# Kernel tuning notes

Measured on AMD Instinct MI355X. Metric: run time of the kernel, lower is better.

## Reference

```python
import jax, jax.numpy as jnp
import numpy as np

N, D_IN, H, D_EMB = 2048, 128, 256, 64


def setup_inputs() -> dict:
    key = jax.random.key(0)
    ks = jax.random.split(key, 8)
    x = jax.random.normal(ks[0], (N, D_IN), dtype=jnp.float32)
    adj = jnp.zeros((N, N), dtype=jnp.float32)  # only its last dim is used (eye sizing)
    s = 0.05
    W0 = jax.random.normal(ks[1], (D_IN, H), dtype=jnp.float32) * s
    b0 = jnp.zeros((H,), dtype=jnp.float32)
    W1 = jax.random.normal(ks[2], (H, D_EMB), dtype=jnp.float32) * s
    b1 = jnp.zeros((D_EMB,), dtype=jnp.float32)
    W2 = jax.random.normal(ks[3], (D_IN, D_IN), dtype=jnp.float32) * s
    b2 = jnp.zeros((D_IN,), dtype=jnp.float32)
    temp = jnp.float32(0.1)
    theta = jnp.float32(0.1)
    return {"x": x, "adj": adj, "W0": W0, "b0": b0, "W1": W1, "b1": b1,
            "W2": W2, "b2": b2, "temp": temp, "theta": theta}


def reference(x, adj, W0, b0, W1, b1, W2, b2, temp, theta):
    # layer 0 (on x) and middle layer 1 (on out_x), both with ReLU activation
    out_x = jax.nn.relu(x @ W0 + b0)            # [N, H]
    emb = jax.nn.relu(out_x @ W1 + b1)          # [N, D_EMB]
    # last layer is applied to the ORIGINAL x (per the `x = model(x)` branch)
    x_last = x @ W2 + b2                        # [N, D_IN]

    # dist[i,j] = -||emb_i - emb_j||^2, computed via the gemm expansion
    sq = jnp.sum(emb * emb, axis=1)             # [N]
    dist = -(sq[:, None] + sq[None, :] - 2.0 * (emb @ emb.T))  # [N, N]

    prob = jax.nn.sigmoid((1.0 + temp) * dist + (5.0 + theta))
    A = prob + jnp.eye(adj.shape[-1], dtype=prob.dtype)        # [N, N]

    # diag(A.sum(-1))^{-1} @ A @ x_last  ==  rowwise divide by degree
    deg = jnp.sum(A, axis=-1)                   # [N]
    out = jax.nn.relu((A @ x_last) / deg[:, None])

    # sigmoid(.) > 0 everywhere, so all N*N entries are nonzero: adj_wts is the
    # full flattened adjacency (data-independent shape, jit-safe)
    adj_wts = A.reshape(-1)
    return out, adj_wts
```

## Files before the change

kernel.cpp:

```cpp
#include <hip/hip_runtime.h>
#include <hip/hip_bf16.h>


typedef short bf16x8 __attribute__((ext_vector_type(8)));
typedef float f32x4 __attribute__((ext_vector_type(4)));

__device__ __forceinline__ unsigned short f2bf(float f) {
    unsigned u = __float_as_uint(f);
    unsigned r = u + 0x7fffu + ((u >> 16) & 1u);
    return (unsigned short)(r >> 16);
}

__device__ __forceinline__ bf16x8 pack_rne8(const float* p) {
    union { unsigned u[4]; bf16x8 v; } r;
    #pragma unroll
    for (int i = 0; i < 4; ++i) {
        unsigned lo = __float_as_uint(p[2 * i]) + 0x8000u;
        unsigned hi = __float_as_uint(p[2 * i + 1]) + 0x8000u;
        r.u[i] = __builtin_amdgcn_perm(hi, lo, 0x07060302u);
    }
    return r.v;
}

__device__ __forceinline__ bf16x8 pack_bf8(const float* p) {
    union { unsigned u[4]; bf16x8 v; } r;
    #pragma unroll
    for (int i = 0; i < 4; ++i)
        r.u[i] = __builtin_amdgcn_perm(__float_as_uint(p[2 * i + 1]),
                                       __float_as_uint(p[2 * i]), 0x07060302u);
    return r.v;
}

__global__ __launch_bounds__(256) void k1_mfma(
    const float* __restrict__ x,
    const float* __restrict__ W0, const float* __restrict__ b0,
    const float* __restrict__ W1, const float* __restrict__ b1,
    const float* __restrict__ W2, const float* __restrict__ b2,
    unsigned short* __restrict__ emb_bf,
    unsigned short* __restrict__ xlT_bf,
    float* __restrict__ sq)
{
    constexpr int LDO = 264;
    __shared__ unsigned short oxb[16 * LDO];
    __shared__ float sqs[4][16];

    const int t = threadIdx.x;
    const int lane = t & 63;
    const int w = t >> 6;
    const int m = lane & 15;
    const int q = lane >> 4;
    const int i0 = blockIdx.x * 16;

    bf16x8 ax[4];
    #pragma unroll
    for (int kb = 0; kb < 4; ++kb) {
        float xf[8];
        *(f32x4*)&xf[0] = *(const f32x4*)(x + (size_t)(i0 + m) * 128 + kb * 32 + q * 8);
        *(f32x4*)&xf[4] = *(const f32x4*)(x + (size_t)(i0 + m) * 128 + kb * 32 + q * 8 + 4);
        ax[kb] = pack_rne8(xf);
    }

    #pragma unroll
    for (int hh = 0; hh < 4; ++hh) {
        const int h = (w * 4 + hh) * 16 + m;
        float bb = b0[h];
        f32x4 acc = {bb, bb, bb, bb};
        #pragma unroll
        for (int kb = 0; kb < 4; ++kb) {
            float wf[8];
            #pragma unroll
            for (int j = 0; j < 8; ++j) wf[j] = W0[(size_t)(kb * 32 + q * 8 + j) * 256 + h];
            acc = __builtin_amdgcn_mfma_f32_16x16x32_bf16(ax[kb], pack_rne8(wf), acc, 0, 0, 0);
        }
        #pragma unroll
        for (int r = 0; r < 4; ++r)
            oxb[(q * 4 + r) * LDO + h] = f2bf(fmaxf(acc[r], 0.0f));
    }
    __syncthreads();

    {
        const int h = w * 16 + m;
        float bb = b1[h];
        f32x4 acc = {bb, bb, bb, bb};
        #pragma unroll
        for (int kb = 0; kb < 8; ++kb) {
            bf16x8 af = *(const bf16x8*)(&oxb[m * LDO + kb * 32 + q * 8]);
            float wf[8];
            #pragma unroll
            for (int j = 0; j < 8; ++j) wf[j] = W1[(size_t)(kb * 32 + q * 8 + j) * 64 + h];
            acc = __builtin_amdgcn_mfma_f32_16x16x32_bf16(af, pack_rne8(wf), acc, 0, 0, 0);
        }
        float s2[4];
        #pragma unroll
        for (int r = 0; r < 4; ++r) {
            float e = fmaxf(acc[r], 0.0f);
            emb_bf[(size_t)(i0 + q * 4 + r) * 64 + h] = f2bf(e);
            s2[r] = e * e;
        }
        #pragma unroll
        for (int r = 0; r < 4; ++r) {
            float v = s2[r];
            v += __shfl_xor(v, 1);
            v += __shfl_xor(v, 2);
            v += __shfl_xor(v, 4);
            v += __shfl_xor(v, 8);
            if (m == 0) sqs[w][q * 4 + r] = v;
        }
    }

    #pragma unroll
    for (int hh = 0; hh < 2; ++hh) {
        const int c = (w * 2 + hh) * 16 + m;
        float bb = b2[c];
        f32x4 acc = {bb, bb, bb, bb};
        #pragma unroll
        for (int kb = 0; kb < 4; ++kb) {
            float wf[8];
            #pragma unroll
            for (int j = 0; j < 8; ++j) wf[j] = W2[(size_t)(kb * 32 + q * 8 + j) * 128 + c];
            acc = __builtin_amdgcn_mfma_f32_16x16x32_bf16(ax[kb], pack_rne8(wf), acc, 0, 0, 0);
        }
        uint2 pk;
        pk.x = (unsigned)f2bf(acc[0]) | ((unsigned)f2bf(acc[1]) << 16);
        pk.y = (unsigned)f2bf(acc[2]) | ((unsigned)f2bf(acc[3]) << 16);
        *(uint2*)(&xlT_bf[(size_t)c * 2048 + i0 + q * 4]) = pk;
    }
    __syncthreads();
    if (t < 16)
        sq[i0 + t] = sqs[0][t] + sqs[1][t] + sqs[2][t] + sqs[3][t];
}

__global__ __launch_bounds__(256) void k2f(
    const unsigned short* __restrict__ emb_bf,
    const unsigned short* __restrict__ xlT_bf,
    const float* __restrict__ sq,
    const float* __restrict__ tempp, const float* __restrict__ thetap,
    float* __restrict__ adjw,
    float* __restrict__ outPart,
    float* __restrict__ degPart)
{
    constexpr int LDP = 132;
    __shared__ float Pt[2][16 * LDP];
    __shared__ float degS[4][16];

    const int t = threadIdx.x;
    const int lane = t & 63;
    const int w = t >> 6;
    const int m = lane & 15;
    const int q = lane >> 4;
    const int i0 = blockIdx.x * 16;
    const int bj = blockIdx.y;
    const int jstrip0 = bj * 256;
    const float scale = 1.0f + tempp[0];
    const float bias = 5.0f + thetap[0];

    bf16x8 a0 = *(const bf16x8*)(emb_bf + (size_t)(i0 + m) * 64 + q * 8);
    bf16x8 a1 = *(const bf16x8*)(emb_bf + (size_t)(i0 + m) * 64 + 32 + q * 8);
    float sqIr[4];
    #pragma unroll
    for (int r = 0; r < 4; ++r) sqIr[r] = sq[i0 + q * 4 + r];

    f32x4 accO0 = {0.f, 0.f, 0.f, 0.f};
    f32x4 accO1 = {0.f, 0.f, 0.f, 0.f};
    float dega[4] = {0.f, 0.f, 0.f, 0.f};
    const int cg = w * 32;

    #pragma unroll
    for (int jt = 0; jt < 2; ++jt) {
        const int j0 = jstrip0 + jt * 128;
        float* P = &Pt[jt][0];

        #pragma unroll
        for (int s = 0; s < 2; ++s) {
            const int col = (w * 2 + s) * 16 + m;
            const unsigned short* ebj = emb_bf + (size_t)(j0 + col) * 64;
            bf16x8 b0 = *(const bf16x8*)(ebj + q * 8);
            bf16x8 b1 = *(const bf16x8*)(ebj + 32 + q * 8);
            f32x4 S = {0.f, 0.f, 0.f, 0.f};
            S = __builtin_amdgcn_mfma_f32_16x16x32_bf16(a0, b0, S, 0, 0, 0);
            S = __builtin_amdgcn_mfma_f32_16x16x32_bf16(a1, b1, S, 0, 0, 0);

            const float csqJ = sq[j0 + col];
            const int gcol = j0 + col;
            #pragma unroll
            for (int r = 0; r < 4; ++r) {
                int grow = i0 + q * 4 + r;
                float dist = 2.0f * S[r] - sqIr[r] - csqJ;
                float z = scale * dist + bias;
                float p = 1.0f / (1.0f + __expf(-z));
                if (grow == gcol) p += 1.0f;
                dega[r] += p;
                P[(q * 4 + r) * LDP + col] = p;
            }
        }
        __syncthreads();

        {
            int row = t >> 4;
            int c0 = (t & 15) * 8;
            f32x4 v0 = *(const f32x4*)(&P[row * LDP + c0]);
            f32x4 v1 = *(const f32x4*)(&P[row * LDP + c0 + 4]);
            f32x4* dst = (f32x4*)(adjw + (size_t)(i0 + row) * 2048 + j0 + c0);
            __builtin_nontemporal_store(v0, dst);
            __builtin_nontemporal_store(v1, dst + 1);
        }

        #pragma unroll
        for (int s = 0; s < 4; ++s) {
            float af[8];
            *(f32x4*)(&af[0]) = *(const f32x4*)(&P[m * LDP + s * 32 + q * 8]);
            *(f32x4*)(&af[4]) = *(const f32x4*)(&P[m * LDP + s * 32 + q * 8 + 4]);
            bf16x8 aa = pack_bf8(af);
            const int k = j0 + s * 32 + q * 8;
            bf16x8 b0 = *(const bf16x8*)(xlT_bf + (size_t)(cg + m) * 2048 + k);
            bf16x8 b1 = *(const bf16x8*)(xlT_bf + (size_t)(cg + 16 + m) * 2048 + k);
            accO0 = __builtin_amdgcn_mfma_f32_16x16x32_bf16(aa, b0, accO0, 0, 0, 0);
            accO1 = __builtin_amdgcn_mfma_f32_16x16x32_bf16(aa, b1, accO1, 0, 0, 0);
        }
    }

    #pragma unroll
    for (int r = 0; r < 4; ++r) {
        float v = dega[r];
        v += __shfl_xor(v, 1);
        v += __shfl_xor(v, 2);
        v += __shfl_xor(v, 4);
        v += __shfl_xor(v, 8);
        if (m == 0) degS[w][q * 4 + r] = v;
    }
    __syncthreads();
    if (t < 16)
        degPart[bj * 2048 + i0 + t] =
            degS[0][t] + degS[1][t] + degS[2][t] + degS[3][t];

    float* op = outPart + ((size_t)bj * 2048 + i0) * 128;
    #pragma unroll
    for (int r = 0; r < 4; ++r) {
        op[(q * 4 + r) * 128 + cg + m] = accO0[r];
        op[(q * 4 + r) * 128 + cg + 16 + m] = accO1[r];
    }
}

__global__ __launch_bounds__(256) void k3_fin(
    const float* __restrict__ outPart, const float* __restrict__ degPart,
    float* __restrict__ out)
{
    int idx4 = (blockIdx.x * 256 + threadIdx.x) * 4;
    int row = idx4 >> 7;
    float4 s = make_float4(0.f, 0.f, 0.f, 0.f);
    float d = 0.f;
    #pragma unroll
    for (int p = 0; p < 8; ++p) {
        float4 v = *(const float4*)(&outPart[(size_t)p * 262144 + idx4]);
        s.x += v.x; s.y += v.y; s.z += v.z; s.w += v.w;
        d += degPart[p * 2048 + row];
    }
    float dinv = 1.0f / d;
    s.x = fmaxf(s.x * dinv, 0.f);
    s.y = fmaxf(s.y * dinv, 0.f);
    s.z = fmaxf(s.z * dinv, 0.f);
    s.w = fmaxf(s.w * dinv, 0.f);
    *(float4*)(&out[idx4]) = s;
}

extern "C" void kernel_launch(void* const* d_in, const int* in_sizes, int n_in,
                              void* d_out, int out_size, void* d_ws, size_t ws_size,
                              hipStream_t stream) {
    const float* x     = (const float*)d_in[0];
    const float* W0    = (const float*)d_in[2];
    const float* b0    = (const float*)d_in[3];
    const float* W1    = (const float*)d_in[4];
    const float* b1    = (const float*)d_in[5];
    const float* W2    = (const float*)d_in[6];
    const float* b2    = (const float*)d_in[7];
    const float* temp  = (const float*)d_in[8];
    const float* theta = (const float*)d_in[9];

    char* ws = (char*)d_ws;
    unsigned short* emb_bf = (unsigned short*)(ws);
    unsigned short* xlT_bf = (unsigned short*)(ws + 262144);
    float* sq      = (float*)(ws + 786432);
    float* degPart = (float*)(ws + 794624);
    float* outPart = (float*)(ws + 860160);

    float* out  = (float*)d_out;
    float* adjw = (float*)d_out + 262144;

    k1_mfma<<<128, 256, 0, stream>>>(x, W0, b0, W1, b1, W2, b2,
                                     emb_bf, xlT_bf, sq);
    k2f<<<dim3(128, 8), 256, 0, stream>>>(emb_bf, xlT_bf, sq, temp, theta,
                                          adjw, outPart, degPart);
    k3_fin<<<256, 256, 0, stream>>>(outPart, degPart, out);
}
```

Baseline: 113.4 us.

## Fuse final reduction into k2 via last-block atomic counter; widen k1 to 512 threads

Removes the separate k3_fin launch by having the last of the eight column-strip blocks for each row tile (found through an atomic counter zeroed in k1) sum the partial outputs and degrees and write the normalized ReLU output. k1 now runs eight waves per block: layer-0 work is split across all waves, and the W1 and W2 GEMMs run on separate wave groups so they proceed concurrently. This trades one kernel launch plus a full pass over outPart for threadfence and atomic overhead at the tail of k2, and it depends on k1 resetting the counters before every run.

```diff
diff --git a/kernel.cpp b/kernel.cpp
--- a/kernel.cpp
+++ b/kernel.cpp
@@ -31,14 +31,15 @@
     return r.v;
 }
 
-__global__ __launch_bounds__(256) void k1_mfma(
+__global__ __launch_bounds__(512) void k1_mfma(
     const float* __restrict__ x,
     const float* __restrict__ W0, const float* __restrict__ b0,
     const float* __restrict__ W1, const float* __restrict__ b1,
     const float* __restrict__ W2, const float* __restrict__ b2,
     unsigned short* __restrict__ emb_bf,
     unsigned short* __restrict__ xlT_bf,
-    float* __restrict__ sq)
+    float* __restrict__ sq,
+    int* __restrict__ cnt)
 {
     constexpr int LDO = 264;
     __shared__ unsigned short oxb[16 * LDO];
@@ -51,6 +52,8 @@
     const int q = lane >> 4;
     const int i0 = blockIdx.x * 16;
 
+    if (blockIdx.x == 0 && t < 128) cnt[t] = 0;
+
     bf16x8 ax[4];
     #pragma unroll
     for (int kb = 0; kb < 4; ++kb) {
@@ -61,8 +64,8 @@
     }
 
     #pragma unroll
-    for (int hh = 0; hh < 4; ++hh) {
-        const int h = (w * 4 + hh) * 16 + m;
+    for (int hh = 0; hh < 2; ++hh) {
+        const int h = (w * 2 + hh) * 16 + m;
         float bb = b0[h];
         f32x4 acc = {bb, bb, bb, bb};
         #pragma unroll
@@ -78,7 +81,7 @@
     }
     __syncthreads();
 
-    {
+    if (w < 4) {
         const int h = w * 16 + m;
         float bb = b1[h];
         f32x4 acc = {bb, bb, bb, bb};
@@ -106,24 +109,25 @@
             v += __shfl_xor(v, 8);
             if (m == 0) sqs[w][q * 4 + r] = v;
         }
-    }
-
-    #pragma unroll
-    for (int hh = 0; hh < 2; ++hh) {
-        const int c = (w * 2 + hh) * 16 + m;
-        float bb = b2[c];
-        f32x4 acc = {bb, bb, bb, bb};
-        #pragma unroll
-        for (int kb = 0; kb < 4; ++kb) {
-            float wf[8];
-            #pragma unroll
-            for (int j = 0; j < 8; ++j) wf[j] = W2[(size_t)(kb * 32 + q * 8 + j) * 128 + c];
-            acc = __builtin_amdgcn_mfma_f32_16x16x32_bf16(ax[kb], pack_rne8(wf), acc, 0, 0, 0);
-        }
-        uint2 pk;
-        pk.x = (unsigned)f2bf(acc[0]) | ((unsigned)f2bf(acc[1]) << 16);
-        pk.y = (unsigned)f2bf(acc[2]) | ((unsigned)f2bf(acc[3]) << 16);
-        *(uint2*)(&xlT_bf[(size_t)c * 2048 + i0 + q * 4]) = pk;
+    } else {
+        const int w2 = w - 4;
+        #pragma unroll
+        for (int hh = 0; hh < 2; ++hh) {
+            const int c = (w2 * 2 + hh) * 16 + m;
+            float bb = b2[c];
+            f32x4 acc = {bb, bb, bb, bb};
+            #pragma unroll
+            for (int kb = 0; kb < 4; ++kb) {
+                float wf[8];
+                #pragma unroll
+                for (int j = 0; j < 8; ++j) wf[j] = W2[(size_t)(kb * 32 + q * 8 + j) * 128 + c];
+                acc = __builtin_amdgcn_mfma_f32_16x16x32_bf16(ax[kb], pack_rne8(wf), acc, 0, 0, 0);
+            }
+            uint2 pk;
+            pk.x = (unsigned)f2bf(acc[0]) | ((unsigned)f2bf(acc[1]) << 16);
+            pk.y = (unsigned)f2bf(acc[2]) | ((unsigned)f2bf(acc[3]) << 16);
+            *(uint2*)(&xlT_bf[(size_t)c * 2048 + i0 + q * 4]) = pk;
+        }
     }
     __syncthreads();
     if (t < 16)
@@ -137,18 +141,23 @@
     const float* __restrict__ tempp, const float* __restrict__ thetap,
     float* __restrict__ adjw,
     float* __restrict__ outPart,
-    float* __restrict__ degPart)
+    float* __restrict__ degPart,
+    int* __restrict__ cnt,
+    float* __restrict__ out)
 {
     constexpr int LDP = 132;
     __shared__ float Pt[2][16 * LDP];
     __shared__ float degS[4][16];
+    __shared__ float dinvS[16];
+    __shared__ int lastFlag;
 
     const int t = threadIdx.x;
     const int lane = t & 63;
     const int w = t >> 6;
     const int m = lane & 15;
     const int q = lane >> 4;
-    const int i0 = blockIdx.x * 16;
+    const int bi = blockIdx.x;
+    const int i0 = bi * 16;
     const int bj = blockIdx.y;
     const int jstrip0 = bj * 256;
     const float scale = 1.0f + tempp[0];
@@ -239,28 +248,45 @@
         op[(q * 4 + r) * 128 + cg + m] = accO0[r];
         op[(q * 4 + r) * 128 + cg + 16 + m] = accO1[r];
     }
-}
-
-__global__ __launch_bounds__(256) void k3_fin(
-    const float* __restrict__ outPart, const float* __restrict__ degPart,
-    float* __restrict__ out)
-{
-    int idx4 = (blockIdx.x * 256 + threadIdx.x) * 4;
-    int row = idx4 >> 7;
-    float4 s = make_float4(0.f, 0.f, 0.f, 0.f);
-    float d = 0.f;
-    #pragma unroll
-    for (int p = 0; p < 8; ++p) {
-        float4 v = *(const float4*)(&outPart[(size_t)p * 262144 + idx4]);
-        s.x += v.x; s.y += v.y; s.z += v.z; s.w += v.w;
-        d += degPart[p * 2048 + row];
-    }
-    float dinv = 1.0f / d;
-    s.x = fmaxf(s.x * dinv, 0.f);
-    s.y = fmaxf(s.y * dinv, 0.f);
-    s.z = fmaxf(s.z * dinv, 0.f);
-    s.w = fmaxf(s.w * dinv, 0.f);
-    *(float4*)(&out[idx4]) = s;
+
+    __threadfence();
+    __syncthreads();
+    if (t == 0) {
+        int old = atomicAdd(&cnt[bi], 1);
+        lastFlag = (old == 7);
+    }
+    __syncthreads();
+    if (lastFlag) {
+        __threadfence();
+        if (t < 16) {
+            float d = 0.f;
+            #pragma unroll
+            for (int p = 0; p < 8; ++p) d += degPart[p * 2048 + i0 + t];
+            dinvS[t] = 1.0f / d;
+        }
+        __syncthreads();
+        const int base = t * 8;
+        const int row = base >> 7;
+        const int col = base & 127;
+        float4 s0 = make_float4(0.f, 0.f, 0.f, 0.f);
+        float4 s1 = make_float4(0.f, 0.f, 0.f, 0.f);
+        #pragma unroll
+        for (int p = 0; p < 8; ++p) {
+            const float* src = outPart + ((size_t)p * 2048 + i0 + row) * 128 + col;
+            float4 a = *(const float4*)(src);
+            float4 b = *(const float4*)(src + 4);
+            s0.x += a.x; s0.y += a.y; s0.z += a.z; s0.w += a.w;
+            s1.x += b.x; s1.y += b.y; s1.z += b.z; s1.w += b.w;
+        }
+        float dinv = dinvS[row];
+        s0.x = fmaxf(s0.x * dinv, 0.f); s0.y = fmaxf(s0.y * dinv, 0.f);
+        s0.z = fmaxf(s0.z * dinv, 0.f); s0.w = fmaxf(s0.w * dinv, 0.f);
+        s1.x = fmaxf(s1.x * dinv, 0.f); s1.y = fmaxf(s1.y * dinv, 0.f);
+        s1.z = fmaxf(s1.z * dinv, 0.f); s1.w = fmaxf(s1.w * dinv, 0.f);
+        float* dst = out + (size_t)(i0 + row) * 128 + col;
+        *(float4*)(dst) = s0;
+        *(float4*)(dst + 4) = s1;
+    }
 }
 
 extern "C" void kernel_launch(void* const* d_in, const int* in_sizes, int n_in,
@@ -281,14 +307,14 @@
     unsigned short* xlT_bf = (unsigned short*)(ws + 262144);
     float* sq      = (float*)(ws + 786432);
     float* degPart = (float*)(ws + 794624);
-    float* outPart = (float*)(ws + 860160);
+    int*   cnt     = (int*)(ws + 860160);
+    float* outPart = (float*)(ws + 861184);
 
     float* out  = (float*)d_out;
     float* adjw = (float*)d_out + 262144;
 
-    k1_mfma<<<128, 256, 0, stream>>>(x, W0, b0, W1, b1, W2, b2,
-                                     emb_bf, xlT_bf, sq);
+    k1_mfma<<<128, 512, 0, stream>>>(x, W0, b0, W1, b1, W2, b2,
+                                     emb_bf, xlT_bf, sq, cnt);
     k2f<<<dim3(128, 8), 256, 0, stream>>>(emb_bf, xlT_bf, sq, temp, theta,
-                                          adjw, outPart, degPart);
-    k3_fin<<<256, 256, 0, stream>>>(outPart, degPart, out);
-}
+                                          adjw, outPart, degPart, cnt, out);
+}
```

Result: slower. 277.8 us (+145.0%).
